# Optimization experiments

Hardware: AMD Instinct MI355X
Metric: run time of the kernel (lower is better)

## Reference

```python
import jax, jax.numpy as jnp
import numpy as np

EPS_STAB = 1e-9   # numerical_stabilizer default
BN_EPS = 1e-5     # flax BatchNorm default epsilon


def setup_inputs() -> dict:
    key = jax.random.key(0)
    ks = jax.random.split(key, 5)
    B, N, C = 2, 4096, 512
    s = 1.0 / np.sqrt(C)
    d = {"inputs": jax.random.normal(ks[0], (B, N, C), jnp.float32)}
    # 1x1 convs == pointwise linear maps [C_in, C_out] + bias
    for i, w in enumerate(["Wq", "Wk", "Wv", "Wo"]):
        d[w] = jax.random.normal(ks[1 + i], (C, C), jnp.float32) * s
    for b in ["bq", "bk", "bv", "bo"]:
        d[b] = jnp.zeros((C,), jnp.float32)
    # BatchNorm (inference: use_running_average=True since train=False)
    d["bn_scale"] = jnp.ones((C,), jnp.float32)
    d["bn_bias"] = jnp.zeros((C,), jnp.float32)
    d["bn_mean"] = jnp.zeros((C,), jnp.float32)
    d["bn_var"] = jnp.ones((C,), jnp.float32)
    return d


def reference(inputs, Wq, bq, Wk, bk, Wv, bv, Wo, bo,
              bn_scale, bn_bias, bn_mean, bn_var):
    # QKV via 1x1 conv == dense projection. [B, N, C]
    q = inputs @ Wq + bq
    k = inputs @ Wk + bk
    v = inputs @ Wv + bv
    # scores [B, M, N]; softmax over last axis (N)
    att = jax.nn.softmax(jnp.einsum('bmc,bnc->bmn', q, k), axis=-1)
    # non-standard renorm: divide by column sums (axis=1 == M axis)
    att = att / (EPS_STAB + jnp.sum(att, axis=1, keepdims=True))
    # faithful to einsum '...MN,...NC->...NC': sum attention over M, scale v
    out = v * jnp.sum(att, axis=1)[..., None]
    # output 1x1 conv
    out = out @ Wo + bo
    # BatchNorm with running stats (feature axis -1)
    out = (out - bn_mean) * jax.lax.rsqrt(bn_var + BN_EPS) * bn_scale + bn_bias
    return jax.nn.relu(out) + inputs
```

## Files before the change

### kernel.cpp

```cpp
#include <hip/hip_runtime.h>
#include <hip/hip_bf16.h>

typedef unsigned short u16;
typedef __attribute__((ext_vector_type(8))) short short8;
typedef __attribute__((ext_vector_type(4))) float f32x4;

__device__ __forceinline__ u16 f2bf(float f) {
    union { float f; unsigned u; } v; v.f = f;
    unsigned r = v.u + 0x7fffu + ((v.u >> 16) & 1u);
    return (u16)(r >> 16);
}

__device__ __forceinline__ float fexp2(float x) {
#if __has_builtin(__builtin_amdgcn_exp2f)
    return __builtin_amdgcn_exp2f(x);
#else
    return __expf(x * 0.6931471805599453f);
#endif
}

__device__ __forceinline__ void async_cp16(const u16* g, u16* l) {
    __builtin_amdgcn_global_load_lds(
        (const __attribute__((address_space(1))) void*)g,
        (__attribute__((address_space(3))) void*)l, 16, 0, 0);
}


__device__ __forceinline__ void gemm512(const u16* __restrict__ A,
                                        const u16* __restrict__ B,
                                        u16* As, u16* Bs,
                                        f32x4 acc[4][4], int tid) {
    const int lane = tid & 63, w = tid >> 6;
    const int quad = lane >> 4, l15 = lane & 15;
    const int wm = tid >> 7, wn = (tid >> 6) & 1;
    const int Gw = lane ^ ((lane >> 3) & 7);
    const int srow = Gw >> 2;
    const int scol = (Gw & 3) * 8;
    const int arow0 = w * 32 + srow, arow1 = arow0 + 16;
    u16* la0 = As + (w * 2 + 0) * 512;
    u16* la1 = As + (w * 2 + 1) * 512;
    u16* lb0 = Bs + (w * 2 + 0) * 512;
    u16* lb1 = Bs + (w * 2 + 1) * 512;
    const int Pr8 = ((l15 * 4 + quad) ^ (l15 >> 1)) * 8;
    for (int k0 = 0; k0 < 512; k0 += 32) {
        __syncthreads();
        async_cp16(A + (size_t)arow0 * 512 + k0 + scol, la0);
        async_cp16(A + (size_t)arow1 * 512 + k0 + scol, la1);
        async_cp16(B + (size_t)arow0 * 512 + k0 + scol, lb0);
        async_cp16(B + (size_t)arow1 * 512 + k0 + scol, lb1);
        __syncthreads();
        short8 af[4], bfr[4];
#pragma unroll
        for (int i = 0; i < 4; i++)
            af[i] = *(const short8*)&As[(wm * 64 + i * 16) * 32 + Pr8];
#pragma unroll
        for (int j = 0; j < 4; j++)
            bfr[j] = *(const short8*)&Bs[(wn * 64 + j * 16) * 32 + Pr8];
#pragma unroll
        for (int i = 0; i < 4; i++)
#pragma unroll
            for (int j = 0; j < 4; j++)
                acc[i][j] = __builtin_amdgcn_mfma_f32_16x16x32_bf16(
                    af[i], bfr[j], acc[i][j], 0, 0, 0);
    }
}

__device__ __forceinline__ void gemm512_r64(const u16* __restrict__ A,
                                            const u16* __restrict__ B,
                                            u16* As, u16* Bs,
                                            f32x4 acc[2][4], int tid) {
    const int lane = tid & 63, w = tid >> 6;
    const int quad = lane >> 4, l15 = lane & 15;
    const int wm = tid >> 7, wn = (tid >> 6) & 1;
    const int Gw = lane ^ ((lane >> 3) & 7);
    const int srow = Gw >> 2;
    const int scol = (Gw & 3) * 8;
    const int arowA = w * 16 + srow;
    const int arowB0 = (w * 2 + 0) * 16 + srow;
    const int arowB1 = (w * 2 + 1) * 16 + srow;
    u16* la = As + w * 512;
    u16* lb0 = Bs + (w * 2 + 0) * 512;
    u16* lb1 = Bs + (w * 2 + 1) * 512;
    const int Pr8 = ((l15 * 4 + quad) ^ (l15 >> 1)) * 8;
    for (int k0 = 0; k0 < 512; k0 += 32) {
        __syncthreads();
        async_cp16(A + (size_t)arowA * 512 + k0 + scol, la);
        async_cp16(B + (size_t)arowB0 * 512 + k0 + scol, lb0);
        async_cp16(B + (size_t)arowB1 * 512 + k0 + scol, lb1);
        __syncthreads();
        short8 af[2], bfr[4];
#pragma unroll
        for (int i = 0; i < 2; i++)
            af[i] = *(const short8*)&As[(wm * 32 + i * 16) * 32 + Pr8];
#pragma unroll
        for (int j = 0; j < 4; j++)
            bfr[j] = *(const short8*)&Bs[(wn * 64 + j * 16) * 32 + Pr8];
#pragma unroll
        for (int i = 0; i < 2; i++)
#pragma unroll
            for (int j = 0; j < 4; j++)
                acc[i][j] = __builtin_amdgcn_mfma_f32_16x16x32_bf16(
                    af[i], bfr[j], acc[i][j], 0, 0, 0);
    }
}

__global__ void prep(const float* __restrict__ X, const float* __restrict__ W0,
                     const float* __restrict__ W1, const float* __restrict__ W2,
                     const float* __restrict__ W3, u16* __restrict__ Xb,
                     u16* __restrict__ T0, u16* __restrict__ T1,
                     u16* __restrict__ T2, u16* __restrict__ T3) {
    __shared__ float tile[32][33];
    int id = blockIdx.x, tid = threadIdx.x;
    if (id < 4096) {
        int idx = (id * 256 + tid) * 4;
        float4 v = *(const float4*)&X[idx];
        ushort4 o;
        o.x = f2bf(v.x); o.y = f2bf(v.y); o.z = f2bf(v.z); o.w = f2bf(v.w);
        *(ushort4*)&Xb[idx] = o;
        return;
    }
    int t = id - 4096;
    int z = t >> 8, rem = t & 255;
    int bo_ = (rem & 15) * 32, bi = (rem >> 4) * 32;
    const float* src; u16* dst;
    switch (z) {
        case 0: src = W0; dst = T0; break;
        case 1: src = W1; dst = T1; break;
        case 2: src = W2; dst = T2; break;
        default: src = W3; dst = T3; break;
    }
    int tx = tid & 31, ty = tid >> 5;
#pragma unroll
    for (int s = 0; s < 4; s++) {
        int i = bi + ty + s * 8;
        tile[ty + s * 8][tx] = src[i * 512 + bo_ + tx];
    }
    __syncthreads();
#pragma unroll
    for (int s = 0; s < 4; s++) {
        int o = bo_ + ty + s * 8;
        dst[o * 512 + bi + tx] = f2bf(tile[tx][ty + s * 8]);
    }
}

__global__ __launch_bounds__(256) void gemm_qkv(
    const u16* __restrict__ Xb, const u16* __restrict__ Wall,
    const float* __restrict__ bq, const float* __restrict__ bk,
    const float* __restrict__ bv, u16* __restrict__ Qall) {
    __shared__ __align__(16) u16 As[128 * 32];
    __shared__ __align__(16) u16 Bs[128 * 32];
    int tid = threadIdx.x;
    int m0 = blockIdx.x * 128, n0 = blockIdx.y * 128, z = blockIdx.z;
    const u16* Bt = Wall + (size_t)z * 262144 + (size_t)n0 * 512;
    const float* bias = (z == 0) ? bq : (z == 1) ? bk : bv;
    const float qs = (z == 0) ? 1.44269504088896340736f : 1.0f;
    u16* C = Qall + (size_t)z * 4194304;
    f32x4 acc[4][4];
#pragma unroll
    for (int i = 0; i < 4; i++)
#pragma unroll
        for (int j = 0; j < 4; j++) acc[i][j] = (f32x4){0.f, 0.f, 0.f, 0.f};
    gemm512(Xb + (size_t)m0 * 512, Bt, As, Bs, acc, tid);
    int lane = tid & 63, quad = lane >> 4, l15 = lane & 15;
    int wm = tid >> 7, wn = (tid >> 6) & 1;
#pragma unroll
    for (int j = 0; j < 4; j++) {
        int n = n0 + wn * 64 + j * 16 + l15;
        float bvv = bias[n];
#pragma unroll
        for (int i = 0; i < 4; i++)
#pragma unroll
            for (int rg = 0; rg < 4; rg++) {
                int m = m0 + wm * 64 + i * 16 + quad * 4 + rg;
                C[(size_t)m * 512 + n] = f2bf((acc[i][j][rg] + bvv) * qs);
            }
    }
}

__global__ __launch_bounds__(256) void attn_pass1(
    const u16* __restrict__ Qb, const u16* __restrict__ Kb,
    float2* __restrict__ statsP) {
    __shared__ __align__(16) u16 As[128 * 32];
    __shared__ __align__(16) u16 Bs[128 * 32];
    int tid = threadIdx.x;
    int mblk = blockIdx.x, nch = blockIdx.y, b = blockIdx.z;
    const u16* Q = Qb + ((size_t)(b * 4096 + mblk * 128)) * 512;
    int lane = tid & 63, quad = lane >> 4, l15 = lane & 15;
    int wm = tid >> 7, wn = (tid >> 6) & 1;
    float runM[4][4], runL[4][4];
#pragma unroll
    for (int i = 0; i < 4; i++)
#pragma unroll
        for (int rg = 0; rg < 4; rg++) { runM[i][rg] = -INFINITY; runL[i][rg] = 0.f; }
    for (int nt = 0; nt < 2; nt++) {
        const u16* K = Kb + ((size_t)(b * 4096 + nch * 256 + nt * 128)) * 512;
        f32x4 acc[4][4];
#pragma unroll
        for (int i = 0; i < 4; i++)
#pragma unroll
            for (int j = 0; j < 4; j++) acc[i][j] = (f32x4){0.f, 0.f, 0.f, 0.f};
        gemm512(Q, K, As, Bs, acc, tid);
#pragma unroll
        for (int i = 0; i < 4; i++)
#pragma unroll
            for (int rg = 0; rg < 4; rg++) {
                float v0 = acc[i][0][rg], v1 = acc[i][1][rg];
                float v2 = acc[i][2][rg], v3 = acc[i][3][rg];
                float vm = fmaxf(fmaxf(v0, v1), fmaxf(v2, v3));
                float mo = runM[i][rg];
                if (vm > mo - 30.f) {
                    float nm = fmaxf(mo, vm);
                    runL[i][rg] = runL[i][rg] * fexp2(mo - nm) +
                                  fexp2(v0 - nm) + fexp2(v1 - nm) +
                                  fexp2(v2 - nm) + fexp2(v3 - nm);
                    runM[i][rg] = nm;
                }
            }
    }
#pragma unroll
    for (int i = 0; i < 4; i++)
#pragma unroll
        for (int rg = 0; rg < 4; rg++) {
            float M = runM[i][rg];
            float Mf = M;
#pragma unroll
            for (int d = 1; d < 16; d <<= 1) Mf = fmaxf(Mf, __shfl_xor(Mf, d));
            float L = runL[i][rg] * fexp2(M - Mf);
#pragma unroll
            for (int d = 1; d < 16; d <<= 1) L += __shfl_xor(L, d);
            if (l15 == 0)
                statsP[((size_t)(b * 32 + nch * 2 + wn)) * 4096 +
                       mblk * 128 + wm * 64 + i * 16 + quad * 4 + rg] =
                    make_float2(Mf, L);
        }
}

__global__ void reduce_stats(const float2* __restrict__ statsP,
                             float* __restrict__ cstat, float* __restrict__ Sg) {
    int t = blockIdx.x * 256 + threadIdx.x;
    int b = t >> 12, m = t & 4095;
    float M = -INFINITY;
    float2 p[32];
#pragma unroll
    for (int ch = 0; ch < 32; ch++) {
        p[ch] = statsP[((size_t)(b * 32 + ch)) * 4096 + m];
        M = fmaxf(M, p[ch].x);
    }
    float L = 0.f;
#pragma unroll
    for (int ch = 0; ch < 32; ch++) L += p[ch].y * fexp2(p[ch].x - M);
    cstat[t] = M + __log2f(L);
    Sg[t] = 0.f;
}

__global__ __launch_bounds__(256) void attn_pass2(
    const u16* __restrict__ Qb, const u16* __restrict__ Kb,
    const float* __restrict__ cstat, float* __restrict__ Sg) {
    __shared__ __align__(16) u16 As[128 * 32];
    __shared__ __align__(16) u16 Bs[128 * 32];
    int tid = threadIdx.x;
    int nblk = blockIdx.x, mch = blockIdx.y, b = blockIdx.z;
    const u16* K = Kb + ((size_t)(b * 4096 + nblk * 128)) * 512;
    int lane = tid & 63, quad = lane >> 4, l15 = lane & 15;
    int wm = tid >> 7, wn = (tid >> 6) & 1;
    float cp0 = 0.f, cp1 = 0.f, cp2 = 0.f, cp3 = 0.f;
    for (int mt = 0; mt < 2; mt++) {
        int m0 = mch * 256 + mt * 128;
        const u16* Q = Qb + ((size_t)(b * 4096 + m0)) * 512;
        f32x4 acc[4][4];
#pragma unroll
        for (int i = 0; i < 4; i++)
#pragma unroll
            for (int j = 0; j < 4; j++) acc[i][j] = (f32x4){0.f, 0.f, 0.f, 0.f};
        gemm512(Q, K, As, Bs, acc, tid);
        float4 c4[4];
#pragma unroll
        for (int i = 0; i < 4; i++)
            c4[i] = *(const float4*)&cstat[b * 4096 + m0 + wm * 64 + i * 16 + quad * 4];
#pragma unroll
        for (int i = 0; i < 4; i++) {
            float cc[4] = {c4[i].x, c4[i].y, c4[i].z, c4[i].w};
#pragma unroll
            for (int rg = 0; rg < 4; rg++) {
                float c = cc[rg];
                float v0 = acc[i][0][rg] - c, v1 = acc[i][1][rg] - c;
                float v2 = acc[i][2][rg] - c, v3 = acc[i][3][rg] - c;
                float vm = fmaxf(fmaxf(v0, v1), fmaxf(v2, v3));
                if (vm > -60.f) {
                    cp0 += fexp2(v0); cp1 += fexp2(v1);
                    cp2 += fexp2(v2); cp3 += fexp2(v3);
                }
            }
        }
    }
    float cps[4] = {cp0, cp1, cp2, cp3};
#pragma unroll
    for (int j = 0; j < 4; j++) {
        float s = cps[j];
        s += __shfl_xor(s, 16);
        s += __shfl_xor(s, 32);
        if (lane < 16)
            atomicAdd(&Sg[b * 4096 + nblk * 128 + wn * 64 + j * 16 + lane], s);
    }
}

__global__ __launch_bounds__(256) void gemm_final(
    const u16* __restrict__ A, const u16* __restrict__ Bt,
    const float* __restrict__ Sg, const float* __restrict__ bo,
    const float* __restrict__ g, const float* __restrict__ bb,
    const float* __restrict__ mean, const float* __restrict__ var,
    const float* __restrict__ X, float* __restrict__ out) {
    __shared__ __align__(16) u16 As[64 * 32];
    __shared__ __align__(16) u16 Bs[128 * 32];
    int tid = threadIdx.x;
    int m0 = blockIdx.x * 64, n0 = blockIdx.y * 128;
    f32x4 acc[2][4];
#pragma unroll
    for (int i = 0; i < 2; i++)
#pragma unroll
        for (int j = 0; j < 4; j++) acc[i][j] = (f32x4){0.f, 0.f, 0.f, 0.f};
    gemm512_r64(A + (size_t)m0 * 512, Bt + (size_t)n0 * 512, As, Bs, acc, tid);
    int lane = tid & 63, quad = lane >> 4, l15 = lane & 15;
    int wm = tid >> 7, wn = (tid >> 6) & 1;
    float sc[2][4];
#pragma unroll
    for (int i = 0; i < 2; i++) {
        float4 s = *(const float4*)&Sg[m0 + wm * 32 + i * 16 + quad * 4];
        float v[4] = {s.x, s.y, s.z, s.w};
#pragma unroll
        for (int rg = 0; rg < 4; rg++) sc[i][rg] = v[rg] / (1e-9f + v[rg]);
    }
#pragma unroll
    for (int j = 0; j < 4; j++) {
        int n = n0 + wn * 64 + j * 16 + l15;
        float aj = rsqrtf(var[n] + 1e-5f) * g[n];
        float cj = bb[n] - mean[n] * aj;
        float bj = bo[n];
#pragma unroll
        for (int i = 0; i < 2; i++)
#pragma unroll
            for (int rg = 0; rg < 4; rg++) {
                int m = m0 + wm * 32 + i * 16 + quad * 4 + rg;
                float x = acc[i][j][rg] * sc[i][rg] + bj;
                float y = x * aj + cj;
                out[(size_t)m * 512 + n] = fmaxf(y, 0.f) + X[(size_t)m * 512 + n];
            }
    }
}

extern "C" void kernel_launch(void* const* d_in, const int* in_sizes, int n_in,
                              void* d_out, int out_size, void* d_ws, size_t ws_size,
                              hipStream_t stream) {
    const float* X  = (const float*)d_in[0];
    const float* Wq = (const float*)d_in[1];
    const float* Wk = (const float*)d_in[2];
    const float* Wv = (const float*)d_in[3];
    const float* Wo = (const float*)d_in[4];
    const float* bq = (const float*)d_in[5];
    const float* bk = (const float*)d_in[6];
    const float* bv = (const float*)d_in[7];
    const float* bo = (const float*)d_in[8];
    const float* g    = (const float*)d_in[9];
    const float* bb   = (const float*)d_in[10];
    const float* mean = (const float*)d_in[11];
    const float* var  = (const float*)d_in[12];
    float* out = (float*)d_out;

    char* ws = (char*)d_ws;
    u16* Xb  = (u16*)(ws + 0);
    u16* Wqt = (u16*)(ws + 8388608);
    u16* Wkt = (u16*)(ws + 8912896);
    u16* Wvt = (u16*)(ws + 9437184);
    u16* Wot = (u16*)(ws + 9961472);
    u16* Qb  = (u16*)(ws + 10485760);
    u16* Kb  = (u16*)(ws + 18874368);
    u16* Vb  = (u16*)(ws + 27262976);
    float2* statsP = (float2*)(ws + 35651584);
    float* cstat   = (float*)(ws + 37748736);
    float* Sg      = (float*)(ws + 37781504);

    prep<<<5120, 256, 0, stream>>>(X, Wq, Wk, Wv, Wo, Xb, Wqt, Wkt, Wvt, Wot);
    gemm_qkv<<<dim3(64, 4, 3), 256, 0, stream>>>(Xb, Wqt, bq, bk, bv, Qb);
    attn_pass1<<<dim3(32, 16, 2), 256, 0, stream>>>(Qb, Kb, statsP);
    reduce_stats<<<32, 256, 0, stream>>>(statsP, cstat, Sg);
    attn_pass2<<<dim3(32, 16, 2), 256, 0, stream>>>(Qb, Kb, cstat, Sg);
    gemm_final<<<dim3(128, 4), 256, 0, stream>>>(Vb, Wot, Sg, bo, g, bb, mean, var,
                                                 X, out);
}
```

Baseline: 231.4 us.

## Store bf16 softmax tiles in pass one and replace QK recompute with column-sum pass

The first attention pass now writes locally normalized exp tiles as packed bf16 to a large workspace buffer, along with per-64-column tile stats. A reduction kernel turns these into per-row correction factors, and a new streaming colsum kernel multiplies the stored tiles by the factors and accumulates column sums atomically. This removes the second QK^T GEMM at the cost of writing and reading about 64 MB of intermediate probabilities and of extra bf16 rounding. The legacy recompute path is kept as a fallback when the workspace is too small.

Measured after the change: 269.4 us. 1.16x slower.

```diff
diff --git a/kernel.cpp b/kernel.cpp
--- a/kernel.cpp
+++ b/kernel.cpp
@@ -2,6 +2,7 @@
 #include <hip/hip_bf16.h>
 
 typedef unsigned short u16;
+typedef unsigned int u32;
 typedef __attribute__((ext_vector_type(8))) short short8;
 typedef __attribute__((ext_vector_type(4))) float f32x4;
 
@@ -9,6 +10,10 @@
     union { float f; unsigned u; } v; v.f = f;
     unsigned r = v.u + 0x7fffu + ((v.u >> 16) & 1u);
     return (u16)(r >> 16);
+}
+__device__ __forceinline__ float bf2f(u16 h) {
+    union { unsigned u; float f; } v; v.u = ((unsigned)h) << 16;
+    return v.f;
 }
 
 __device__ __forceinline__ float fexp2(float x) {
@@ -177,7 +182,118 @@
     }
 }
 
-__global__ __launch_bounds__(256) void attn_pass1(
+__global__ __launch_bounds__(256) void attn_pass1p(
+    const u16* __restrict__ Qb, const u16* __restrict__ Kb,
+    float2* __restrict__ statsP, u32* __restrict__ Pbuf, int b0) {
+    __shared__ __align__(16) u16 As[128 * 32];
+    __shared__ __align__(16) u16 Bs[128 * 32];
+    int tid = threadIdx.x;
+    int mblk = blockIdx.x, nch = blockIdx.y, zb = blockIdx.z, b = b0 + zb;
+    const u16* Q = Qb + ((size_t)(b * 4096 + mblk * 128)) * 512;
+    int lane = tid & 63, quad = lane >> 4, l15 = lane & 15;
+    int wm = tid >> 7, wn = (tid >> 6) & 1;
+    for (int nt = 0; nt < 2; nt++) {
+        const u16* K = Kb + ((size_t)(b * 4096 + nch * 256 + nt * 128)) * 512;
+        f32x4 acc[4][4];
+#pragma unroll
+        for (int i = 0; i < 4; i++)
+#pragma unroll
+            for (int j = 0; j < 4; j++) acc[i][j] = (f32x4){0.f, 0.f, 0.f, 0.f};
+        gemm512(Q, K, As, Bs, acc, tid);
+        u32* Pt = Pbuf + (((size_t)(zb * 32 + mblk) * 16 + nch) * 2 + nt) * 8192;
+        int ch = nch * 4 + nt * 2 + wn;
+#pragma unroll
+        for (int i = 0; i < 4; i++)
+#pragma unroll
+            for (int rg = 0; rg < 4; rg++) {
+                float v0 = acc[i][0][rg], v1 = acc[i][1][rg];
+                float v2 = acc[i][2][rg], v3 = acc[i][3][rg];
+                float Mt = fmaxf(fmaxf(v0, v1), fmaxf(v2, v3));
+                Mt = fmaxf(Mt, __shfl_xor(Mt, 1));
+                Mt = fmaxf(Mt, __shfl_xor(Mt, 2));
+                Mt = fmaxf(Mt, __shfl_xor(Mt, 4));
+                Mt = fmaxf(Mt, __shfl_xor(Mt, 8));
+                float p0 = fexp2(v0 - Mt), p1 = fexp2(v1 - Mt);
+                float p2 = fexp2(v2 - Mt), p3 = fexp2(v3 - Mt);
+                float L = p0 + p1 + p2 + p3;
+                L += __shfl_xor(L, 1);
+                L += __shfl_xor(L, 2);
+                L += __shfl_xor(L, 4);
+                L += __shfl_xor(L, 8);
+                Pt[((i * 4 + rg) * 2 + 0) * 256 + tid] =
+                    (u32)f2bf(p0) | ((u32)f2bf(p1) << 16);
+                Pt[((i * 4 + rg) * 2 + 1) * 256 + tid] =
+                    (u32)f2bf(p2) | ((u32)f2bf(p3) << 16);
+                if (l15 == 0)
+                    statsP[((size_t)(b * 64 + ch)) * 4096 + mblk * 128 +
+                           wm * 64 + i * 16 + quad * 4 + rg] =
+                        make_float2(Mt, L);
+            }
+    }
+}
+
+__global__ void reduce_statsF(const float2* __restrict__ statsP,
+                              float* __restrict__ F, float* __restrict__ Sg,
+                              int b0) {
+    int t = blockIdx.x * 256 + threadIdx.x;
+    int b = b0 + (t >> 12), m = t & 4095;
+    float2 p[64];
+    float M = -INFINITY;
+#pragma unroll
+    for (int ch = 0; ch < 64; ch++) {
+        p[ch] = statsP[((size_t)(b * 64 + ch)) * 4096 + m];
+        M = fmaxf(M, p[ch].x);
+    }
+    float Z = 0.f;
+#pragma unroll
+    for (int ch = 0; ch < 64; ch++) Z += p[ch].y * fexp2(p[ch].x - M);
+    float c = M + __log2f(Z);
+#pragma unroll
+    for (int ch = 0; ch < 64; ch++)
+        F[((size_t)(b * 64 + ch)) * 4096 + m] = fexp2(p[ch].x - c);
+    Sg[b * 4096 + m] = 0.f;
+}
+
+__global__ __launch_bounds__(256) void colsum(
+    const u32* __restrict__ Pbuf, const float* __restrict__ F,
+    float* __restrict__ Sg, int b0) {
+    int tid = threadIdx.x, lane = tid & 63;
+    int wm = tid >> 7, wn = (tid >> 6) & 1, quad = lane >> 4;
+    int nch = blockIdx.x, nt = blockIdx.y & 1, mgrp = blockIdx.y >> 1;
+    int zb = blockIdx.z, b = b0 + zb;
+    int ch = nch * 4 + nt * 2 + wn;
+    const float* Fc = F + ((size_t)(b * 64 + ch)) * 4096;
+    float cp[4] = {0.f, 0.f, 0.f, 0.f};
+    for (int mb = 0; mb < 4; mb++) {
+        int mblk = mgrp * 4 + mb;
+        const u32* Pt =
+            Pbuf + (((size_t)(zb * 32 + mblk) * 16 + nch) * 2 + nt) * 8192;
+#pragma unroll
+        for (int i = 0; i < 4; i++) {
+            float4 Fv = *(const float4*)&Fc[mblk * 128 + wm * 64 + i * 16 + quad * 4];
+            float fv[4] = {Fv.x, Fv.y, Fv.z, Fv.w};
+#pragma unroll
+            for (int rg = 0; rg < 4; rg++) {
+                u32 ua = Pt[((i * 4 + rg) * 2 + 0) * 256 + tid];
+                u32 ub = Pt[((i * 4 + rg) * 2 + 1) * 256 + tid];
+                cp[0] += bf2f((u16)(ua & 0xffff)) * fv[rg];
+                cp[1] += bf2f((u16)(ua >> 16)) * fv[rg];
+                cp[2] += bf2f((u16)(ub & 0xffff)) * fv[rg];
+                cp[3] += bf2f((u16)(ub >> 16)) * fv[rg];
+            }
+        }
+    }
+#pragma unroll
+    for (int j = 0; j < 4; j++) {
+        float s = cp[j];
+        s += __shfl_xor(s, 16);
+        s += __shfl_xor(s, 32);
+        if (lane < 16)
+            atomicAdd(&Sg[b * 4096 + nch * 256 + nt * 128 + wn * 64 + j * 16 + lane], s);
+    }
+}
+
+__global__ __launch_bounds__(256) void legacy_pass1(
     const u16* __restrict__ Qb, const u16* __restrict__ Kb,
     float2* __restrict__ statsP) {
     __shared__ __align__(16) u16 As[128 * 32];
@@ -235,8 +351,8 @@
         }
 }
 
-__global__ void reduce_stats(const float2* __restrict__ statsP,
-                             float* __restrict__ cstat, float* __restrict__ Sg) {
+__global__ void legacy_reduce(const float2* __restrict__ statsP,
+                              float* __restrict__ cstat, float* __restrict__ Sg) {
     int t = blockIdx.x * 256 + threadIdx.x;
     int b = t >> 12, m = t & 4095;
     float M = -INFINITY;
@@ -253,7 +369,7 @@
     Sg[t] = 0.f;
 }
 
-__global__ __launch_bounds__(256) void attn_pass2(
+__global__ __launch_bounds__(256) void legacy_pass2(
     const u16* __restrict__ Qb, const u16* __restrict__ Kb,
     const float* __restrict__ cstat, float* __restrict__ Sg) {
     __shared__ __align__(16) u16 As[128 * 32];
@@ -261,7 +377,7 @@
     int tid = threadIdx.x;
     int nblk = blockIdx.x, mch = blockIdx.y, b = blockIdx.z;
     const u16* K = Kb + ((size_t)(b * 4096 + nblk * 128)) * 512;
-    int lane = tid & 63, quad = lane >> 4, l15 = lane & 15;
+    int lane = tid & 63, quad = lane >> 4;
     int wm = tid >> 7, wn = (tid >> 6) & 1;
     float cp0 = 0.f, cp1 = 0.f, cp2 = 0.f, cp3 = 0.f;
     for (int mt = 0; mt < 2; mt++) {
@@ -369,21 +485,38 @@
     char* ws = (char*)d_ws;
     u16* Xb  = (u16*)(ws + 0);
     u16* Wqt = (u16*)(ws + 8388608);
-    u16* Wkt = (u16*)(ws + 8912896);
-    u16* Wvt = (u16*)(ws + 9437184);
     u16* Wot = (u16*)(ws + 9961472);
     u16* Qb  = (u16*)(ws + 10485760);
     u16* Kb  = (u16*)(ws + 18874368);
     u16* Vb  = (u16*)(ws + 27262976);
     float2* statsP = (float2*)(ws + 35651584);
-    float* cstat   = (float*)(ws + 37748736);
-    float* Sg      = (float*)(ws + 37781504);
-
-    prep<<<5120, 256, 0, stream>>>(X, Wq, Wk, Wv, Wo, Xb, Wqt, Wkt, Wvt, Wot);
+    float* F       = (float*)(ws + 39845888);
+    float* Sg      = (float*)(ws + 41943040);
+    float* cstat   = (float*)(ws + 41975808);
+    u32* Pbuf      = (u32*)(ws + 42008576);
+
+    const size_t FULL_NEED  = 42008576ull + 67108864ull;
+    const size_t BATCH_NEED = 42008576ull + 33554432ull;
+
+    prep<<<5120, 256, 0, stream>>>(X, Wq, Wk, Wv, Wo, Xb, Wqt, Wqt + 262144,
+                                   Wqt + 524288, Wot);
     gemm_qkv<<<dim3(64, 4, 3), 256, 0, stream>>>(Xb, Wqt, bq, bk, bv, Qb);
-    attn_pass1<<<dim3(32, 16, 2), 256, 0, stream>>>(Qb, Kb, statsP);
-    reduce_stats<<<32, 256, 0, stream>>>(statsP, cstat, Sg);
-    attn_pass2<<<dim3(32, 16, 2), 256, 0, stream>>>(Qb, Kb, cstat, Sg);
+
+    if (ws_size >= FULL_NEED) {
+        attn_pass1p<<<dim3(32, 16, 2), 256, 0, stream>>>(Qb, Kb, statsP, Pbuf, 0);
+        reduce_statsF<<<32, 256, 0, stream>>>(statsP, F, Sg, 0);
+        colsum<<<dim3(16, 16, 2), 256, 0, stream>>>(Pbuf, F, Sg, 0);
+    } else if (ws_size >= BATCH_NEED) {
+        for (int b = 0; b < 2; b++) {
+            attn_pass1p<<<dim3(32, 16, 1), 256, 0, stream>>>(Qb, Kb, statsP, Pbuf, b);
+            reduce_statsF<<<16, 256, 0, stream>>>(statsP, F, Sg, b);
+            colsum<<<dim3(16, 16, 1), 256, 0, stream>>>(Pbuf, F, Sg, b);
+        }
+    } else {
+        legacy_pass1<<<dim3(32, 16, 2), 256, 0, stream>>>(Qb, Kb, statsP);
+        legacy_reduce<<<32, 256, 0, stream>>>(statsP, cstat, Sg);
+        legacy_pass2<<<dim3(32, 16, 2), 256, 0, stream>>>(Qb, Kb, cstat, Sg);
+    }
     gemm_final<<<dim3(128, 4), 256, 0, stream>>>(Vb, Wot, Sg, bo, g, bb, mean, var,
                                                  X, out);
 }
```

## Fuse attention passes with grid barrier and FP8-cached probabilities

Applied to the files above, without the earlier changes.

Merges the two attention passes and the stats reduction into one kernel. Each block keeps its exponentiated score tile in registers as packed FP8, waits at a grid-wide atomic counter barrier, reduces the row log-sum-exp stats from global memory, then rescales the cached probabilities to build column sums. This drops the second full QK^T GEMM and two kernel launches. In exchange it relies on all 1024 blocks being co-resident (hence launch_bounds 256,4), the barrier has a spin timeout that could silently give wrong results, and FP8 storage of probabilities adds quantisation error.

Result: slower. 373.5 us (+61.4%).

```diff
diff --git a/kernel.cpp b/kernel.cpp
--- a/kernel.cpp
+++ b/kernel.cpp
@@ -2,6 +2,7 @@
 #include <hip/hip_bf16.h>
 
 typedef unsigned short u16;
+typedef unsigned int u32;
 typedef __attribute__((ext_vector_type(8))) short short8;
 typedef __attribute__((ext_vector_type(4))) float f32x4;
 
@@ -18,6 +19,48 @@
     return __expf(x * 0.6931471805599453f);
 #endif
 }
+
+#if __has_builtin(__builtin_amdgcn_cvt_pk_fp8_f32) && \
+    __has_builtin(__builtin_amdgcn_cvt_f32_fp8)
+#define FP8_HW 1
+#else
+#define FP8_HW 0
+#endif
+
+#if !FP8_HW
+__device__ __forceinline__ u32 sw_fp8(float x) {
+    union { float f; u32 u; } v; v.f = x;
+    int E = (int)(v.u >> 23) - 127;
+    if (x < 0.001953125f) return 0;
+    if (E < -6) return (u32)(x * 512.0f + 0.5f);
+    u32 m = v.u & 0x7fffffu;
+    u32 r = (m + 0x80000u) >> 20;
+    u32 bits = ((u32)(E + 7) << 3) + r;
+    return bits > 0x7eu ? 0x7eu : bits;
+}
+__device__ __forceinline__ float sw_fp8d(u32 b) {
+    u32 e = (b >> 3) & 15u, m = b & 7u;
+    if (e == 0) return (float)m * 0.001953125f;
+    union { u32 u; float f; } v; v.u = ((e + 120u) << 23) | (m << 20);
+    return v.f;
+}
+#endif
+
+__device__ __forceinline__ u32 fp8x4_pack(float p0, float p1, float p2, float p3) {
+#if FP8_HW
+    u32 v = (u32)__builtin_amdgcn_cvt_pk_fp8_f32(p0, p1, 0, false);
+    v = (u32)__builtin_amdgcn_cvt_pk_fp8_f32(p2, p3, (int)v, true);
+    return v;
+#else
+    return sw_fp8(p0) | (sw_fp8(p1) << 8) | (sw_fp8(p2) << 16) | (sw_fp8(p3) << 24);
+#endif
+}
+
+#if FP8_HW
+#define FP8_DEC(v, s) __builtin_amdgcn_cvt_f32_fp8((int)(v), (s))
+#else
+#define FP8_DEC(v, s) sw_fp8d(((v) >> ((s) * 8)) & 0xffu)
+#endif
 
 __device__ __forceinline__ void async_cp16(const u16* g, u16* l) {
     __builtin_amdgcn_global_load_lds(
@@ -108,9 +151,17 @@
                      const float* __restrict__ W1, const float* __restrict__ W2,
                      const float* __restrict__ W3, u16* __restrict__ Xb,
                      u16* __restrict__ T0, u16* __restrict__ T1,
-                     u16* __restrict__ T2, u16* __restrict__ T3) {
+                     u16* __restrict__ T2, u16* __restrict__ T3,
+                     float* __restrict__ Sg, u32* __restrict__ counter) {
     __shared__ float tile[32][33];
     int id = blockIdx.x, tid = threadIdx.x;
+    if (id == 5120) {
+        if (tid == 0) *counter = 0;
+        float4 z = {0.f, 0.f, 0.f, 0.f};
+#pragma unroll
+        for (int t = 0; t < 8; t++) ((float4*)Sg)[tid + t * 256] = z;
+        return;
+    }
     if (id < 4096) {
         int idx = (id * 256 + tid) * 4;
         float4 v = *(const float4*)&X[idx];
@@ -177,21 +228,21 @@
     }
 }
 
-__global__ __launch_bounds__(256) void attn_pass1(
+__global__ __launch_bounds__(256, 4) void attn_fused(
     const u16* __restrict__ Qb, const u16* __restrict__ Kb,
-    float2* __restrict__ statsP) {
+    float2* __restrict__ statsP, float* __restrict__ Sg,
+    u32* __restrict__ counter) {
     __shared__ __align__(16) u16 As[128 * 32];
     __shared__ __align__(16) u16 Bs[128 * 32];
+    __shared__ float mtbuf[2][2][128];
+    __shared__ float cbuf[128];
     int tid = threadIdx.x;
     int mblk = blockIdx.x, nch = blockIdx.y, b = blockIdx.z;
     const u16* Q = Qb + ((size_t)(b * 4096 + mblk * 128)) * 512;
     int lane = tid & 63, quad = lane >> 4, l15 = lane & 15;
     int wm = tid >> 7, wn = (tid >> 6) & 1;
-    float runM[4][4], runL[4][4];
-#pragma unroll
-    for (int i = 0; i < 4; i++)
-#pragma unroll
-        for (int rg = 0; rg < 4; rg++) { runM[i][rg] = -INFINITY; runL[i][rg] = 0.f; }
+    u32 P[2][16];
+#pragma unroll
     for (int nt = 0; nt < 2; nt++) {
         const u16* K = Kb + ((size_t)(b * 4096 + nch * 256 + nt * 128)) * 512;
         f32x4 acc[4][4];
@@ -200,108 +251,94 @@
 #pragma unroll
             for (int j = 0; j < 4; j++) acc[i][j] = (f32x4){0.f, 0.f, 0.f, 0.f};
         gemm512(Q, K, As, Bs, acc, tid);
+        int ch = nch * 4 + nt * 2 + wn;
 #pragma unroll
         for (int i = 0; i < 4; i++)
 #pragma unroll
             for (int rg = 0; rg < 4; rg++) {
                 float v0 = acc[i][0][rg], v1 = acc[i][1][rg];
                 float v2 = acc[i][2][rg], v3 = acc[i][3][rg];
-                float vm = fmaxf(fmaxf(v0, v1), fmaxf(v2, v3));
-                float mo = runM[i][rg];
-                if (vm > mo - 30.f) {
-                    float nm = fmaxf(mo, vm);
-                    runL[i][rg] = runL[i][rg] * fexp2(mo - nm) +
-                                  fexp2(v0 - nm) + fexp2(v1 - nm) +
-                                  fexp2(v2 - nm) + fexp2(v3 - nm);
-                    runM[i][rg] = nm;
+                float Mt = fmaxf(fmaxf(v0, v1), fmaxf(v2, v3));
+                Mt = fmaxf(Mt, __shfl_xor(Mt, 1));
+                Mt = fmaxf(Mt, __shfl_xor(Mt, 2));
+                Mt = fmaxf(Mt, __shfl_xor(Mt, 4));
+                Mt = fmaxf(Mt, __shfl_xor(Mt, 8));
+                float e8 = Mt - 8.0f;
+                float p0 = fexp2(v0 - e8), p1 = fexp2(v1 - e8);
+                float p2 = fexp2(v2 - e8), p3 = fexp2(v3 - e8);
+                P[nt][i * 4 + rg] = fp8x4_pack(p0, p1, p2, p3);
+                float L = p0 + p1 + p2 + p3;
+                L += __shfl_xor(L, 1);
+                L += __shfl_xor(L, 2);
+                L += __shfl_xor(L, 4);
+                L += __shfl_xor(L, 8);
+                if (l15 == 0) {
+                    int r = wm * 64 + i * 16 + quad * 4 + rg;
+                    statsP[((size_t)(b * 64 + ch)) * 4096 + mblk * 128 + r] =
+                        make_float2(Mt, L * 0.00390625f);
+                    mtbuf[nt][wn][r] = Mt;
                 }
             }
     }
-#pragma unroll
-    for (int i = 0; i < 4; i++)
-#pragma unroll
-        for (int rg = 0; rg < 4; rg++) {
-            float M = runM[i][rg];
-            float Mf = M;
-#pragma unroll
-            for (int d = 1; d < 16; d <<= 1) Mf = fmaxf(Mf, __shfl_xor(Mf, d));
-            float L = runL[i][rg] * fexp2(M - Mf);
-#pragma unroll
-            for (int d = 1; d < 16; d <<= 1) L += __shfl_xor(L, d);
-            if (l15 == 0)
-                statsP[((size_t)(b * 32 + nch * 2 + wn)) * 4096 +
-                       mblk * 128 + wm * 64 + i * 16 + quad * 4 + rg] =
-                    make_float2(Mf, L);
+    __syncthreads();
+    __threadfence();
+    if (tid == 0) {
+        __hip_atomic_fetch_add(counter, 1u, __ATOMIC_ACQ_REL,
+                               __HIP_MEMORY_SCOPE_AGENT);
+        int it = 0;
+        while (__hip_atomic_load(counter, __ATOMIC_ACQUIRE,
+                                 __HIP_MEMORY_SCOPE_AGENT) < 1024u &&
+               it < (1 << 24)) {
+            __builtin_amdgcn_s_sleep(2);
+            ++it;
         }
-}
-
-__global__ void reduce_stats(const float2* __restrict__ statsP,
-                             float* __restrict__ cstat, float* __restrict__ Sg) {
-    int t = blockIdx.x * 256 + threadIdx.x;
-    int b = t >> 12, m = t & 4095;
-    float M = -INFINITY;
-    float2 p[32];
-#pragma unroll
-    for (int ch = 0; ch < 32; ch++) {
-        p[ch] = statsP[((size_t)(b * 32 + ch)) * 4096 + m];
-        M = fmaxf(M, p[ch].x);
-    }
-    float L = 0.f;
-#pragma unroll
-    for (int ch = 0; ch < 32; ch++) L += p[ch].y * fexp2(p[ch].x - M);
-    cstat[t] = M + __log2f(L);
-    Sg[t] = 0.f;
-}
-
-__global__ __launch_bounds__(256) void attn_pass2(
-    const u16* __restrict__ Qb, const u16* __restrict__ Kb,
-    const float* __restrict__ cstat, float* __restrict__ Sg) {
-    __shared__ __align__(16) u16 As[128 * 32];
-    __shared__ __align__(16) u16 Bs[128 * 32];
-    int tid = threadIdx.x;
-    int nblk = blockIdx.x, mch = blockIdx.y, b = blockIdx.z;
-    const u16* K = Kb + ((size_t)(b * 4096 + nblk * 128)) * 512;
-    int lane = tid & 63, quad = lane >> 4, l15 = lane & 15;
-    int wm = tid >> 7, wn = (tid >> 6) & 1;
-    float cp0 = 0.f, cp1 = 0.f, cp2 = 0.f, cp3 = 0.f;
-    for (int mt = 0; mt < 2; mt++) {
-        int m0 = mch * 256 + mt * 128;
-        const u16* Q = Qb + ((size_t)(b * 4096 + m0)) * 512;
-        f32x4 acc[4][4];
-#pragma unroll
-        for (int i = 0; i < 4; i++)
-#pragma unroll
-            for (int j = 0; j < 4; j++) acc[i][j] = (f32x4){0.f, 0.f, 0.f, 0.f};
-        gemm512(Q, K, As, Bs, acc, tid);
-        float4 c4[4];
-#pragma unroll
-        for (int i = 0; i < 4; i++)
-            c4[i] = *(const float4*)&cstat[b * 4096 + m0 + wm * 64 + i * 16 + quad * 4];
-#pragma unroll
-        for (int i = 0; i < 4; i++) {
-            float cc[4] = {c4[i].x, c4[i].y, c4[i].z, c4[i].w};
+    }
+    __syncthreads();
+    if (tid < 128) {
+        const float2* sp = statsP + (size_t)b * 64 * 4096 + mblk * 128 + tid;
+        float M = -INFINITY;
+#pragma unroll 4
+        for (int c2 = 0; c2 < 64; c2++) M = fmaxf(M, sp[(size_t)c2 * 4096].x);
+        float Z = 0.f;
+#pragma unroll 4
+        for (int c2 = 0; c2 < 64; c2++) {
+            float2 p = sp[(size_t)c2 * 4096];
+            Z += p.y * fexp2(p.x - M);
+        }
+        cbuf[tid] = M + __log2f(Z);
+    }
+    __syncthreads();
+    float cp[2][4];
+#pragma unroll
+    for (int nt = 0; nt < 2; nt++)
+#pragma unroll
+        for (int j = 0; j < 4; j++) cp[nt][j] = 0.f;
+#pragma unroll
+    for (int nt = 0; nt < 2; nt++)
+#pragma unroll
+        for (int i = 0; i < 4; i++)
 #pragma unroll
             for (int rg = 0; rg < 4; rg++) {
-                float c = cc[rg];
-                float v0 = acc[i][0][rg] - c, v1 = acc[i][1][rg] - c;
-                float v2 = acc[i][2][rg] - c, v3 = acc[i][3][rg] - c;
-                float vm = fmaxf(fmaxf(v0, v1), fmaxf(v2, v3));
-                if (vm > -60.f) {
-                    cp0 += fexp2(v0); cp1 += fexp2(v1);
-                    cp2 += fexp2(v2); cp3 += fexp2(v3);
-                }
+                int r = wm * 64 + i * 16 + quad * 4 + rg;
+                float F = fexp2(mtbuf[nt][wn][r] - 8.0f - cbuf[r]);
+                u32 e = P[nt][i * 4 + rg];
+                cp[nt][0] += FP8_DEC(e, 0) * F;
+                cp[nt][1] += FP8_DEC(e, 1) * F;
+                cp[nt][2] += FP8_DEC(e, 2) * F;
+                cp[nt][3] += FP8_DEC(e, 3) * F;
             }
+#pragma unroll
+    for (int nt = 0; nt < 2; nt++)
+#pragma unroll
+        for (int j = 0; j < 4; j++) {
+            float s = cp[nt][j];
+            s += __shfl_xor(s, 16);
+            s += __shfl_xor(s, 32);
+            if (lane < 16)
+                atomicAdd(&Sg[b * 4096 + nch * 256 + nt * 128 + wn * 64 +
+                              j * 16 + lane],
+                          s);
         }
-    }
-    float cps[4] = {cp0, cp1, cp2, cp3};
-#pragma unroll
-    for (int j = 0; j < 4; j++) {
-        float s = cps[j];
-        s += __shfl_xor(s, 16);
-        s += __shfl_xor(s, 32);
-        if (lane < 16)
-            atomicAdd(&Sg[b * 4096 + nblk * 128 + wn * 64 + j * 16 + lane], s);
-    }
 }
 
 __global__ __launch_bounds__(256) void gemm_final(
@@ -369,21 +406,18 @@
     char* ws = (char*)d_ws;
     u16* Xb  = (u16*)(ws + 0);
     u16* Wqt = (u16*)(ws + 8388608);
-    u16* Wkt = (u16*)(ws + 8912896);
-    u16* Wvt = (u16*)(ws + 9437184);
     u16* Wot = (u16*)(ws + 9961472);
     u16* Qb  = (u16*)(ws + 10485760);
     u16* Kb  = (u16*)(ws + 18874368);
     u16* Vb  = (u16*)(ws + 27262976);
     float2* statsP = (float2*)(ws + 35651584);
-    float* cstat   = (float*)(ws + 37748736);
-    float* Sg      = (float*)(ws + 37781504);
-
-    prep<<<5120, 256, 0, stream>>>(X, Wq, Wk, Wv, Wo, Xb, Wqt, Wkt, Wvt, Wot);
+    float* Sg      = (float*)(ws + 39845888);
+    u32* counter   = (u32*)(ws + 39878656);
+
+    prep<<<5121, 256, 0, stream>>>(X, Wq, Wk, Wv, Wo, Xb, Wqt, Wqt + 262144,
+                                   Wqt + 524288, Wot, Sg, counter);
     gemm_qkv<<<dim3(64, 4, 3), 256, 0, stream>>>(Xb, Wqt, bq, bk, bv, Qb);
-    attn_pass1<<<dim3(32, 16, 2), 256, 0, stream>>>(Qb, Kb, statsP);
-    reduce_stats<<<32, 256, 0, stream>>>(statsP, cstat, Sg);
-    attn_pass2<<<dim3(32, 16, 2), 256, 0, stream>>>(Qb, Kb, cstat, Sg);
+    attn_fused<<<dim3(32, 16, 2), 256, 0, stream>>>(Qb, Kb, statsP, Sg, counter);
     gemm_final<<<dim3(128, 4), 256, 0, stream>>>(Vb, Wot, Sg, bo, g, bb, mean, var,
                                                  X, out);
 }
```
